# Kernel tuning notes

Hardware: AMD Instinct MI355X
Metric: run time of the kernel (lower is better)

## Reference

```python
import jax, jax.numpy as jnp
import numpy as np

N_TOKEN = 8192
N_EMBED = 512
N_SAMPLE = 10
TAU = 1.0
RHO = 1.0


def setup_inputs() -> dict:
    key = jax.random.key(0)
    k1, k2 = jax.random.split(key)
    inputs = jax.random.normal(k1, (4, 2048, N_EMBED), dtype=jnp.float32)
    embeds = jax.random.normal(k2, (N_TOKEN, N_EMBED), dtype=jnp.float32)
    return {"inputs": inputs, "embeds": embeds}


def reference(inputs, embeds):
    size = inputs.shape
    x = inputs.reshape(-1, N_EMBED)  # (N, D)
    n = x.shape[0]
    # squared distances, scaled by n_token (as in get_distances)
    dists = (jnp.sum(x * x, axis=-1, keepdims=True)
             + jnp.sum(embeds * embeds, axis=-1)[None, :]
             - 2.0 * jnp.matmul(x, embeds.T)) / N_TOKEN  # (N, K)
    logits = -dists / TAU  # categorical(softmax(logits)) == categorical(logits)
    skey = jax.random.fold_in(jax.random.key(0), 1)
    # multinomial with replacement: n_sample i.i.d. categorical draws per row
    samples = jax.random.categorical(skey, logits[:, None, :], axis=-1,
                                     shape=(n, N_SAMPLE))  # (N, n_sample) int
    quantized_embs = embeds[samples].mean(axis=1)  # (N, D) gather + mean
    quantized = x + jax.lax.stop_gradient(quantized_embs - x)  # straight-through
    gkey = jax.random.fold_in(jax.random.key(0), 2)
    gates = jax.random.bernoulli(gkey, RHO, (n,)).astype(x.dtype)[:, None]
    quantized = quantized * gates + (1.0 - gates) * x
    quantized = quantized.reshape(size)
    samples = samples.reshape(size[:-1] + (N_SAMPLE,))
    return quantized, samples
```

## Files before the change

### kernel.cpp

```cpp
#include <hip/hip_runtime.h>
#include <stdint.h>
#include <math.h>

#define N_ROWS 8192
#define N_TOK  8192
#define N_DIM  512
#define N_SAMP 10
#define GK     1536

typedef __attribute__((ext_vector_type(8))) short bf16x8_t;
typedef __attribute__((ext_vector_type(4))) float f32x4_t;

__host__ __device__ __forceinline__ void tf2x32(uint32_t ks0, uint32_t ks1,
                                                uint32_t& x0, uint32_t& x1) {
  uint32_t ks2 = ks0 ^ ks1 ^ 0x1BD11BDAu;
  x0 += ks0; x1 += ks1;
#define TF_ROUND(r) { x0 += x1; x1 = (x1 << (r)) | (x1 >> (32 - (r))); x1 ^= x0; }
  TF_ROUND(13) TF_ROUND(15) TF_ROUND(26) TF_ROUND(6)
  x0 += ks1; x1 += ks2 + 1u;
  TF_ROUND(17) TF_ROUND(29) TF_ROUND(16) TF_ROUND(24)
  x0 += ks2; x1 += ks0 + 2u;
  TF_ROUND(13) TF_ROUND(15) TF_ROUND(26) TF_ROUND(6)
  x0 += ks0; x1 += ks1 + 3u;
  TF_ROUND(17) TF_ROUND(29) TF_ROUND(16) TF_ROUND(24)
  x0 += ks1; x1 += ks2 + 4u;
  TF_ROUND(13) TF_ROUND(15) TF_ROUND(26) TF_ROUND(6)
  x0 += ks2; x1 += ks0 + 5u;
#undef TF_ROUND
}

__device__ __forceinline__ unsigned short f2bf_rne(float f) {
  uint32_t u = __float_as_uint(f);
  uint32_t r = (u + 0x7fffu + ((u >> 16) & 1u)) >> 16;
  return (unsigned short)r;
}
__device__ __forceinline__ float bf2f(unsigned short h) {
  return __uint_as_float((uint32_t)h << 16);
}

__global__ __launch_bounds__(256) void rownorm_kernel(const float* __restrict__ M,
                                                      float* __restrict__ out) {
  int lane = threadIdx.x & 63;
  int row = (int)((blockIdx.x * blockDim.x + threadIdx.x) >> 6);
  const float* p = M + (size_t)row * N_DIM;
  float acc = 0.f;
#pragma unroll
  for (int d = 0; d < N_DIM; d += 64) {
    float v = p[d + lane];
    acc = fmaf(v, v, acc);
  }
#pragma unroll
  for (int off = 32; off; off >>= 1) acc += __shfl_xor(acc, off, 64);
  if (lane == 0) out[row] = acc;
}

__global__ __launch_bounds__(256) void init_state_kernel(float* __restrict__ rmin,
                                                         int* __restrict__ ridx) {
  int i = blockIdx.x * 256 + threadIdx.x;
  if (i < N_ROWS * N_SAMP) { rmin[i] = INFINITY; ridx[i] = 0; }
}

__global__ __launch_bounds__(256) void split_kernel(const float* __restrict__ src,
                                                    unsigned short* __restrict__ dst,
                                                    int mode) {
  int t = blockIdx.x * 256 + threadIdx.x;
  int row = t >> 7;
  int c = (t & 127) << 2;
  float4 v = *(const float4*)(src + (size_t)row * N_DIM + c);
  ushort4 hi, lo;
  hi.x = f2bf_rne(v.x); lo.x = f2bf_rne(v.x - bf2f(hi.x));
  hi.y = f2bf_rne(v.y); lo.y = f2bf_rne(v.y - bf2f(hi.y));
  hi.z = f2bf_rne(v.z); lo.z = f2bf_rne(v.z - bf2f(hi.z));
  hi.w = f2bf_rne(v.w); lo.w = f2bf_rne(v.w - bf2f(hi.w));
  unsigned short* base = dst + (size_t)row * GK;
  *(ushort4*)(base + c) = hi;
  if (mode == 0) {
    *(ushort4*)(base + 512 + c) = lo;
    *(ushort4*)(base + 1024 + c) = hi;
  } else {
    *(ushort4*)(base + 512 + c) = hi;
    *(ushort4*)(base + 1024 + c) = lo;
  }
}

__device__ __forceinline__ void async_cp16(const void* g, void* l) {
  __builtin_amdgcn_global_load_lds((const __attribute__((address_space(1))) void*)g,
                                   (__attribute__((address_space(3))) void*)l, 16, 0, 0);
}

__global__ __launch_bounds__(256) void gemm_bf16_kernel(const unsigned short* __restrict__ A2,
                                                        const unsigned short* __restrict__ B2,
                                                        const float* __restrict__ xx,
                                                        const float* __restrict__ ee,
                                                        float* __restrict__ E,
                                                        int ks, int KC) {
  __shared__ __align__(16) unsigned short As[128 * 32];
  __shared__ __align__(16) unsigned short Bs[128 * 32];
  int tid = threadIdx.x;
  int w = tid >> 6, l = tid & 63;
  int row0 = blockIdx.y * 128;
  int col0 = blockIdx.x * 128;
  int bcol0 = ks + col0;
  int wm = (w & 1) * 64, wn = (w >> 1) * 64;
  int quad = l >> 4, r15 = l & 15;

  f32x4_t acc[4][4];
#pragma unroll
  for (int i = 0; i < 4; ++i)
#pragma unroll
    for (int j = 0; j < 4; ++j) acc[i][j] = (f32x4_t){0.f, 0.f, 0.f, 0.f};

  int c0 = w * 64 + l;
  int c1 = c0 + 256;
  const size_t ga0 = (size_t)(row0 + (c0 >> 2)) * GK + (c0 & 3) * 8;
  const size_t ga1 = (size_t)(row0 + (c1 >> 2)) * GK + (c1 & 3) * 8;
  const size_t gb0 = (size_t)(bcol0 + (c0 >> 2)) * GK + (c0 & 3) * 8;
  const size_t gb1 = (size_t)(bcol0 + (c1 >> 2)) * GK + (c1 & 3) * 8;

  for (int k0 = 0; k0 < GK; k0 += 32) {
    async_cp16(A2 + ga0 + k0, As + c0 * 8);
    async_cp16(A2 + ga1 + k0, As + c1 * 8);
    async_cp16(B2 + gb0 + k0, Bs + c0 * 8);
    async_cp16(B2 + gb1 + k0, Bs + c1 * 8);
    __syncthreads();

    bf16x8_t af[4], bf[4];
#pragma unroll
    for (int i = 0; i < 4; ++i)
      af[i] = *(const bf16x8_t*)&As[(wm + i * 16 + r15) * 32 + quad * 8];
#pragma unroll
    for (int j = 0; j < 4; ++j)
      bf[j] = *(const bf16x8_t*)&Bs[(wn + j * 16 + r15) * 32 + quad * 8];
#pragma unroll
    for (int i = 0; i < 4; ++i)
#pragma unroll
      for (int j = 0; j < 4; ++j)
        acc[i][j] = __builtin_amdgcn_mfma_f32_16x16x32_bf16(af[i], bf[j], acc[i][j], 0, 0, 0);
    __syncthreads();
  }

  const float inv_nt = 1.f / 8192.f;
  float eev[4];
#pragma unroll
  for (int j = 0; j < 4; ++j) eev[j] = ee[ks + col0 + wn + j * 16 + r15];
#pragma unroll
  for (int i = 0; i < 4; ++i) {
#pragma unroll
    for (int r = 0; r < 4; ++r) {
      int grow = row0 + wm + i * 16 + quad * 4 + r;
      float xxv = xx[grow];
#pragma unroll
      for (int j = 0; j < 4; ++j) {
        int gcol = col0 + wn + j * 16 + r15;
        float dist = (xxv + eev[j] - 2.0f * acc[i][j][r]) * inv_nt;
        E[(size_t)grow * KC + gcol] = expf(dist);
      }
    }
  }
}

__global__ __launch_bounds__(256) void gemm_nt_kernel(const float* __restrict__ A,
                                                      const float* __restrict__ B,
                                                      const float* __restrict__ xx,
                                                      const float* __restrict__ ee,
                                                      float* __restrict__ E,
                                                      int ks, int KC) {
  __shared__ __align__(16) float Asf[32][68];
  __shared__ __align__(16) float Bsf[32][68];
  int tid = threadIdx.x;
  int row0 = blockIdx.y * 64;
  int colB0 = blockIdx.x * 64 + ks;
  int tx = tid & 15, ty = tid >> 4;
  float acc[4][4] = {};
  for (int d0 = 0; d0 < N_DIM; d0 += 32) {
#pragma unroll
    for (int r = 0; r < 2; ++r) {
      int c = tid + 256 * r;
      int m = c >> 3;
      int dv = (c & 7) << 2;
      const float4 va = *(const float4*)(A + (size_t)(row0 + m) * N_DIM + d0 + dv);
      Asf[dv + 0][m] = va.x; Asf[dv + 1][m] = va.y;
      Asf[dv + 2][m] = va.z; Asf[dv + 3][m] = va.w;
      const float4 vb = *(const float4*)(B + (size_t)(colB0 + m) * N_DIM + d0 + dv);
      Bsf[dv + 0][m] = vb.x; Bsf[dv + 1][m] = vb.y;
      Bsf[dv + 2][m] = vb.z; Bsf[dv + 3][m] = vb.w;
    }
    __syncthreads();
#pragma unroll
    for (int dd = 0; dd < 32; ++dd) {
      float4 a4 = *(const float4*)&Asf[dd][ty << 2];
      float4 b4 = *(const float4*)&Bsf[dd][tx << 2];
      float av[4] = {a4.x, a4.y, a4.z, a4.w};
      float bv[4] = {b4.x, b4.y, b4.z, b4.w};
#pragma unroll
      for (int i = 0; i < 4; ++i)
#pragma unroll
        for (int j = 0; j < 4; ++j)
          acc[i][j] = fmaf(av[i], bv[j], acc[i][j]);
    }
    __syncthreads();
  }
  const float inv_nt = 1.f / 8192.f;
  int colC0 = blockIdx.x * 64;
  float eev[4];
#pragma unroll
  for (int j = 0; j < 4; ++j) eev[j] = ee[ks + colC0 + (tx << 2) + j];
#pragma unroll
  for (int i = 0; i < 4; ++i) {
    int grow = row0 + (ty << 2) + i;
    float xxv = xx[grow];
    float4 v;
    v.x = expf((xxv + eev[0] - 2.0f * acc[i][0]) * inv_nt);
    v.y = expf((xxv + eev[1] - 2.0f * acc[i][1]) * inv_nt);
    v.z = expf((xxv + eev[2] - 2.0f * acc[i][2]) * inv_nt);
    v.w = expf((xxv + eev[3] - 2.0f * acc[i][3]) * inv_nt);
    *(float4*)(E + (size_t)grow * KC + colC0 + (tx << 2)) = v;
  }
}

__global__ __launch_bounds__(256) void sample_kernel(const float* __restrict__ E,
                                                     float* __restrict__ rmin,
                                                     int* __restrict__ ridx,
                                                     int ks, int KC,
                                                     uint32_t k0, uint32_t k1) {
  int lane = threadIdx.x & 63;
  int row = (int)((blockIdx.x * blockDim.x + threadIdx.x) >> 6);
  float bmin[N_SAMP];
  int bidx[N_SAMP];
#pragma unroll
  for (int s = 0; s < N_SAMP; ++s) { bmin[s] = INFINITY; bidx[s] = 0; }
  const float tiny = 1.1754943508222875e-38f;
  uint32_t row_c = (uint32_t)row * (uint32_t)N_SAMP * 8192u;

  for (int kk = lane; kk < KC; kk += 64) {
    int k = ks + kk;
    float Ek = E[(size_t)row * KC + kk];
    uint32_t base_c = row_c + (uint32_t)k;
#pragma unroll
    for (int s = 0; s < N_SAMP; ++s) {
      uint32_t x0 = 0u, x1 = base_c + (uint32_t)s * 8192u;
      tf2x32(k0, k1, x0, x1);
      uint32_t bits = x0 ^ x1;
      float u = __uint_as_float(0x3f800000u | (bits >> 9)) - 1.0f;
      u = fmaxf(u, tiny);
      float wv = -logf(u) * Ek;
      if (wv < bmin[s]) { bmin[s] = wv; bidx[s] = k; }
    }
  }
#pragma unroll
  for (int s = 0; s < N_SAMP; ++s) {
    float v = bmin[s];
    int id = bidx[s];
#pragma unroll
    for (int off = 32; off; off >>= 1) {
      float ov = __shfl_xor(v, off, 64);
      int oi = __shfl_xor(id, off, 64);
      if (ov < v || (ov == v && oi < id)) { v = ov; id = oi; }
    }
    if (lane == 0) {
      size_t p = (size_t)row * N_SAMP + s;
      if (v < rmin[p]) { rmin[p] = v; ridx[p] = id; }
    }
  }
}

__global__ __launch_bounds__(256) void gather_kernel(const float* __restrict__ emb,
                                                     const int* __restrict__ ridx,
                                                     const float* __restrict__ x,
                                                     float* __restrict__ outq,
                                                     float* __restrict__ outs) {
  int lane = threadIdx.x & 63;
  int row = (int)((blockIdx.x * blockDim.x + threadIdx.x) >> 6);
  int idx[N_SAMP];
#pragma unroll
  for (int s = 0; s < N_SAMP; ++s) idx[s] = ridx[row * N_SAMP + s];
  if (lane < N_SAMP) outs[row * N_SAMP + lane] = (float)idx[lane];
#pragma unroll
  for (int c = lane; c < N_DIM; c += 64) {
    float sum = 0.f;
#pragma unroll
    for (int s = 0; s < N_SAMP; ++s) sum += emb[(size_t)idx[s] * N_DIM + c];
    float qe = sum / 10.0f;
    float xv = x[(size_t)row * N_DIM + c];
    outq[(size_t)row * N_DIM + c] = xv + (qe - xv);
  }
}

extern "C" void kernel_launch(void* const* d_in, const int* in_sizes, int n_in,
                              void* d_out, int out_size, void* d_ws, size_t ws_size,
                              hipStream_t stream) {
  const float* x = (const float*)d_in[0];
  const float* emb = (const float*)d_in[1];
  float* out_q = (float*)d_out;
  float* out_s = out_q + (size_t)N_ROWS * N_DIM;

  const size_t fixed_f = (size_t)N_ROWS + N_TOK + 2 * (size_t)N_ROWS * N_SAMP;
  const size_t out_f = (size_t)N_ROWS * N_DIM + (size_t)N_ROWS * N_SAMP;
  const size_t split_u = (size_t)N_ROWS * GK;

  uint32_t s0 = 0u, s1 = 1u;
  tf2x32(0u, 0u, s0, s1);

  int KC = 0;
  for (int c = 8192; c >= 128; c >>= 1) {
    size_t need = fixed_f * 4 + 2 * split_u * 2 + (size_t)N_ROWS * c * 4;
    if (need <= ws_size) { KC = c; break; }
  }

  if (KC) {
    float* xx = (float*)d_ws;
    float* ee = xx + N_ROWS;
    float* rmin = ee + N_TOK;
    int* ridx = (int*)(rmin + (size_t)N_ROWS * N_SAMP);
    unsigned short* A2 = (unsigned short*)(ridx + (size_t)N_ROWS * N_SAMP);
    unsigned short* B2 = A2 + split_u;
    float* E = (float*)(B2 + split_u);

    rownorm_kernel<<<2048, 256, 0, stream>>>(x, xx);
    rownorm_kernel<<<2048, 256, 0, stream>>>(emb, ee);
    init_state_kernel<<<(N_ROWS * N_SAMP + 255) / 256, 256, 0, stream>>>(rmin, ridx);
    split_kernel<<<N_ROWS * 128 / 256, 256, 0, stream>>>(x, A2, 0);
    split_kernel<<<N_ROWS * 128 / 256, 256, 0, stream>>>(emb, B2, 1);

    for (int ks = 0; ks < N_TOK; ks += KC) {
      gemm_bf16_kernel<<<dim3(KC / 128, N_ROWS / 128), 256, 0, stream>>>(A2, B2, xx, ee, E, ks, KC);
      sample_kernel<<<2048, 256, 0, stream>>>(E, rmin, ridx, ks, KC, s0, s1);
    }
    gather_kernel<<<2048, 256, 0, stream>>>(emb, ridx, x, out_q, out_s);
    return;
  }

  float *xx, *ee, *rmin, *E;
  int* ridx;
  KC = 0;
  for (int c = 8192; c >= 64; c >>= 1) {
    if ((fixed_f + (size_t)N_ROWS * c) * 4 <= ws_size) { KC = c; break; }
  }
  if (KC) {
    xx = (float*)d_ws;
    ee = xx + N_ROWS;
    rmin = ee + N_TOK;
    ridx = (int*)(rmin + (size_t)N_ROWS * N_SAMP);
    E = (float*)(ridx + (size_t)N_ROWS * N_SAMP);
  } else if (fixed_f * 4 <= ws_size) {
    KC = 512;
    xx = (float*)d_ws;
    ee = xx + N_ROWS;
    rmin = ee + N_TOK;
    ridx = (int*)(rmin + (size_t)N_ROWS * N_SAMP);
    E = out_q;
  } else {
    KC = 256;
    E = out_q;
    float* tail = out_q + (out_f - fixed_f);
    xx = tail;
    ee = xx + N_ROWS;
    rmin = ee + N_TOK;
    ridx = (int*)(rmin + (size_t)N_ROWS * N_SAMP);
  }

  rownorm_kernel<<<2048, 256, 0, stream>>>(x, xx);
  rownorm_kernel<<<2048, 256, 0, stream>>>(emb, ee);
  init_state_kernel<<<(N_ROWS * N_SAMP + 255) / 256, 256, 0, stream>>>(rmin, ridx);
  for (int ks = 0; ks < N_TOK; ks += KC) {
    gemm_nt_kernel<<<dim3(KC / 64, N_ROWS / 64), 256, 0, stream>>>(x, emb, xx, ee, E, ks, KC);
    sample_kernel<<<2048, 256, 0, stream>>>(E, rmin, ridx, ks, KC, s0, s1);
  }
  gather_kernel<<<2048, 256, 0, stream>>>(emb, ridx, x, out_q, out_s);
}
```

Before: 1.724 ms.

## Fuse distance GEMM with Gumbel-style sampling via packed 64-bit atomicMin

Sampling moves into the bf16 MFMA GEMM epilogue. Each tile computes exp(dist), generates the threefry randoms per element, reduces a packed (value,index) 64-bit key across 16 lanes, and merges the winners globally with atomicMin. This removes the 256 MB intermediate E matrix write and read, and launches a single 64x64-tile grid instead of chunked GEMM/sample pairs. In exchange the GEMM blocks carry the heavy RNG and log work in registers, and about 10 atomics per row per column tile contend on the same addresses. Sample indices are now unpacked in a separate kernel before the gather.

```diff
diff --git a/kernel.cpp b/kernel.cpp
--- a/kernel.cpp
+++ b/kernel.cpp
@@ -38,6 +38,13 @@
   return __uint_as_float((uint32_t)h << 16);
 }
 
+__device__ __forceinline__ unsigned long long shfl_xor_u64(unsigned long long v, int off) {
+  uint32_t lo = (uint32_t)v, hi = (uint32_t)(v >> 32);
+  lo = (uint32_t)__shfl_xor((int)lo, off, 64);
+  hi = (uint32_t)__shfl_xor((int)hi, off, 64);
+  return ((unsigned long long)hi << 32) | lo;
+}
+
 __global__ __launch_bounds__(256) void rownorm_kernel(const float* __restrict__ M,
                                                       float* __restrict__ out) {
   int lane = threadIdx.x & 63;
@@ -54,10 +61,9 @@
   if (lane == 0) out[row] = acc;
 }
 
-__global__ __launch_bounds__(256) void init_state_kernel(float* __restrict__ rmin,
-                                                         int* __restrict__ ridx) {
+__global__ __launch_bounds__(256) void init_pack_kernel(unsigned long long* __restrict__ rpack) {
   int i = blockIdx.x * 256 + threadIdx.x;
-  if (i < N_ROWS * N_SAMP) { rmin[i] = INFINITY; ridx[i] = 0; }
+  if (i < N_ROWS * N_SAMP) rpack[i] = 0xFFFFFFFFFFFFFFFFULL;
 }
 
 __global__ __launch_bounds__(256) void split_kernel(const float* __restrict__ src,
@@ -88,19 +94,16 @@
                                    (__attribute__((address_space(3))) void*)l, 16, 0, 0);
 }
 
-__global__ __launch_bounds__(256) void gemm_bf16_kernel(const unsigned short* __restrict__ A2,
-                                                        const unsigned short* __restrict__ B2,
-                                                        const float* __restrict__ xx,
-                                                        const float* __restrict__ ee,
-                                                        float* __restrict__ E,
-                                                        int ks, int KC) {
+__global__ __launch_bounds__(256) void fused_gemm_sample_kernel(
+    const unsigned short* __restrict__ A2, const unsigned short* __restrict__ B2,
+    const float* __restrict__ xx, const float* __restrict__ ee,
+    unsigned long long* __restrict__ rpack, uint32_t k0s, uint32_t k1s) {
   __shared__ __align__(16) unsigned short As[128 * 32];
   __shared__ __align__(16) unsigned short Bs[128 * 32];
   int tid = threadIdx.x;
   int w = tid >> 6, l = tid & 63;
   int row0 = blockIdx.y * 128;
   int col0 = blockIdx.x * 128;
-  int bcol0 = ks + col0;
   int wm = (w & 1) * 64, wn = (w >> 1) * 64;
   int quad = l >> 4, r15 = l & 15;
 
@@ -114,8 +117,8 @@
   int c1 = c0 + 256;
   const size_t ga0 = (size_t)(row0 + (c0 >> 2)) * GK + (c0 & 3) * 8;
   const size_t ga1 = (size_t)(row0 + (c1 >> 2)) * GK + (c1 & 3) * 8;
-  const size_t gb0 = (size_t)(bcol0 + (c0 >> 2)) * GK + (c0 & 3) * 8;
-  const size_t gb1 = (size_t)(bcol0 + (c1 >> 2)) * GK + (c1 & 3) * 8;
+  const size_t gb0 = (size_t)(col0 + (c0 >> 2)) * GK + (c0 & 3) * 8;
+  const size_t gb1 = (size_t)(col0 + (c1 >> 2)) * GK + (c1 & 3) * 8;
 
   for (int k0 = 0; k0 < GK; k0 += 32) {
     async_cp16(A2 + ga0 + k0, As + c0 * 8);
@@ -142,18 +145,51 @@
   const float inv_nt = 1.f / 8192.f;
   float eev[4];
 #pragma unroll
-  for (int j = 0; j < 4; ++j) eev[j] = ee[ks + col0 + wn + j * 16 + r15];
+  for (int j = 0; j < 4; ++j) eev[j] = ee[col0 + wn + j * 16 + r15];
 #pragma unroll
   for (int i = 0; i < 4; ++i) {
 #pragma unroll
     for (int r = 0; r < 4; ++r) {
-      int grow = row0 + wm + i * 16 + quad * 4 + r;
-      float xxv = xx[grow];
-#pragma unroll
-      for (int j = 0; j < 4; ++j) {
-        int gcol = col0 + wn + j * 16 + r15;
-        float dist = (xxv + eev[j] - 2.0f * acc[i][j][r]) * inv_nt;
-        E[(size_t)grow * KC + gcol] = expf(dist);
+      float xxv = xx[row0 + wm + i * 16 + quad * 4 + r];
+#pragma unroll
+      for (int j = 0; j < 4; ++j)
+        acc[i][j][r] = expf((xxv + eev[j] - 2.0f * acc[i][j][r]) * inv_nt);
+    }
+  }
+
+  const float tiny = 1.1754943508222875e-38f;
+  uint32_t kcol[4];
+#pragma unroll
+  for (int j = 0; j < 4; ++j) kcol[j] = (uint32_t)(col0 + wn + j * 16 + r15);
+  int rbase = row0 + wm + quad * 4;
+
+  for (int s = 0; s < N_SAMP; ++s) {
+    uint32_t soff = (uint32_t)s * 8192u;
+#pragma unroll
+    for (int i = 0; i < 4; ++i) {
+#pragma unroll
+      for (int r = 0; r < 4; ++r) {
+        uint32_t rowid = (uint32_t)(rbase + i * 16 + r);
+        uint32_t cbase = rowid * 81920u + soff;
+        unsigned long long b = 0xFFFFFFFFFFFFFFFFULL;
+#pragma unroll
+        for (int j = 0; j < 4; ++j) {
+          uint32_t x0 = 0u, x1 = cbase + kcol[j];
+          tf2x32(k0s, k1s, x0, x1);
+          uint32_t bits = x0 ^ x1;
+          float u = __uint_as_float(0x3f800000u | (bits >> 9)) - 1.0f;
+          u = fmaxf(u, tiny);
+          float wv = -logf(u) * acc[i][j][r];
+          unsigned long long p =
+              ((unsigned long long)__float_as_uint(wv) << 32) | kcol[j];
+          b = (p < b) ? p : b;
+        }
+#pragma unroll
+        for (int off = 1; off < 16; off <<= 1) {
+          unsigned long long ob = shfl_xor_u64(b, off);
+          b = (ob < b) ? ob : b;
+        }
+        if (r15 == 0) atomicMin(&rpack[(size_t)rowid * N_SAMP + s], b);
       }
     }
   }
@@ -219,23 +255,21 @@
 }
 
 __global__ __launch_bounds__(256) void sample_kernel(const float* __restrict__ E,
-                                                     float* __restrict__ rmin,
-                                                     int* __restrict__ ridx,
+                                                     unsigned long long* __restrict__ rpack,
                                                      int ks, int KC,
                                                      uint32_t k0, uint32_t k1) {
   int lane = threadIdx.x & 63;
   int row = (int)((blockIdx.x * blockDim.x + threadIdx.x) >> 6);
-  float bmin[N_SAMP];
-  int bidx[N_SAMP];
-#pragma unroll
-  for (int s = 0; s < N_SAMP; ++s) { bmin[s] = INFINITY; bidx[s] = 0; }
+  unsigned long long best[N_SAMP];
+#pragma unroll
+  for (int s = 0; s < N_SAMP; ++s) best[s] = 0xFFFFFFFFFFFFFFFFULL;
   const float tiny = 1.1754943508222875e-38f;
-  uint32_t row_c = (uint32_t)row * (uint32_t)N_SAMP * 8192u;
+  uint32_t row_c = (uint32_t)row * 81920u;
 
   for (int kk = lane; kk < KC; kk += 64) {
-    int k = ks + kk;
+    uint32_t k = (uint32_t)(ks + kk);
     float Ek = E[(size_t)row * KC + kk];
-    uint32_t base_c = row_c + (uint32_t)k;
+    uint32_t base_c = row_c + k;
 #pragma unroll
     for (int s = 0; s < N_SAMP; ++s) {
       uint32_t x0 = 0u, x1 = base_c + (uint32_t)s * 8192u;
@@ -244,37 +278,37 @@
       float u = __uint_as_float(0x3f800000u | (bits >> 9)) - 1.0f;
       u = fmaxf(u, tiny);
       float wv = -logf(u) * Ek;
-      if (wv < bmin[s]) { bmin[s] = wv; bidx[s] = k; }
+      unsigned long long p = ((unsigned long long)__float_as_uint(wv) << 32) | k;
+      if (p < best[s]) best[s] = p;
     }
   }
 #pragma unroll
   for (int s = 0; s < N_SAMP; ++s) {
-    float v = bmin[s];
-    int id = bidx[s];
+    unsigned long long b = best[s];
 #pragma unroll
     for (int off = 32; off; off >>= 1) {
-      float ov = __shfl_xor(v, off, 64);
-      int oi = __shfl_xor(id, off, 64);
-      if (ov < v || (ov == v && oi < id)) { v = ov; id = oi; }
-    }
-    if (lane == 0) {
-      size_t p = (size_t)row * N_SAMP + s;
-      if (v < rmin[p]) { rmin[p] = v; ridx[p] = id; }
-    }
-  }
+      unsigned long long ob = shfl_xor_u64(b, off);
+      b = (ob < b) ? ob : b;
+    }
+    if (lane == 0) atomicMin(&rpack[(size_t)row * N_SAMP + s], b);
+  }
+}
+
+__global__ __launch_bounds__(256) void unpack_kernel(const unsigned long long* __restrict__ rpack,
+                                                     float* __restrict__ outs) {
+  int i = blockIdx.x * 256 + threadIdx.x;
+  if (i < N_ROWS * N_SAMP) outs[i] = (float)(uint32_t)(rpack[i] & 0xFFFFFFFFu);
 }
 
 __global__ __launch_bounds__(256) void gather_kernel(const float* __restrict__ emb,
-                                                     const int* __restrict__ ridx,
+                                                     const float* __restrict__ outs,
                                                      const float* __restrict__ x,
-                                                     float* __restrict__ outq,
-                                                     float* __restrict__ outs) {
+                                                     float* __restrict__ outq) {
   int lane = threadIdx.x & 63;
   int row = (int)((blockIdx.x * blockDim.x + threadIdx.x) >> 6);
   int idx[N_SAMP];
 #pragma unroll
-  for (int s = 0; s < N_SAMP; ++s) idx[s] = ridx[row * N_SAMP + s];
-  if (lane < N_SAMP) outs[row * N_SAMP + lane] = (float)idx[lane];
+  for (int s = 0; s < N_SAMP; ++s) idx[s] = (int)outs[row * N_SAMP + s];
 #pragma unroll
   for (int c = lane; c < N_DIM; c += 64) {
     float sum = 0.f;
@@ -294,77 +328,65 @@
   float* out_q = (float*)d_out;
   float* out_s = out_q + (size_t)N_ROWS * N_DIM;
 
-  const size_t fixed_f = (size_t)N_ROWS + N_TOK + 2 * (size_t)N_ROWS * N_SAMP;
-  const size_t out_f = (size_t)N_ROWS * N_DIM + (size_t)N_ROWS * N_SAMP;
+  const size_t pack_n = (size_t)N_ROWS * N_SAMP;
+  const size_t fixed_b = (N_ROWS + N_TOK) * 4 + pack_n * 8;
   const size_t split_u = (size_t)N_ROWS * GK;
 
   uint32_t s0 = 0u, s1 = 1u;
   tf2x32(0u, 0u, s0, s1);
 
-  int KC = 0;
-  for (int c = 8192; c >= 128; c >>= 1) {
-    size_t need = fixed_f * 4 + 2 * split_u * 2 + (size_t)N_ROWS * c * 4;
-    if (need <= ws_size) { KC = c; break; }
-  }
-
-  if (KC) {
+  if (fixed_b + 2 * split_u * 2 <= ws_size) {
     float* xx = (float*)d_ws;
     float* ee = xx + N_ROWS;
-    float* rmin = ee + N_TOK;
-    int* ridx = (int*)(rmin + (size_t)N_ROWS * N_SAMP);
-    unsigned short* A2 = (unsigned short*)(ridx + (size_t)N_ROWS * N_SAMP);
+    unsigned long long* rpack = (unsigned long long*)(ee + N_TOK);
+    unsigned short* A2 = (unsigned short*)(rpack + pack_n);
     unsigned short* B2 = A2 + split_u;
-    float* E = (float*)(B2 + split_u);
 
     rownorm_kernel<<<2048, 256, 0, stream>>>(x, xx);
     rownorm_kernel<<<2048, 256, 0, stream>>>(emb, ee);
-    init_state_kernel<<<(N_ROWS * N_SAMP + 255) / 256, 256, 0, stream>>>(rmin, ridx);
+    init_pack_kernel<<<(int)((pack_n + 255) / 256), 256, 0, stream>>>(rpack);
     split_kernel<<<N_ROWS * 128 / 256, 256, 0, stream>>>(x, A2, 0);
     split_kernel<<<N_ROWS * 128 / 256, 256, 0, stream>>>(emb, B2, 1);
 
-    for (int ks = 0; ks < N_TOK; ks += KC) {
-      gemm_bf16_kernel<<<dim3(KC / 128, N_ROWS / 128), 256, 0, stream>>>(A2, B2, xx, ee, E, ks, KC);
-      sample_kernel<<<2048, 256, 0, stream>>>(E, rmin, ridx, ks, KC, s0, s1);
-    }
-    gather_kernel<<<2048, 256, 0, stream>>>(emb, ridx, x, out_q, out_s);
+    fused_gemm_sample_kernel<<<dim3(64, 64), 256, 0, stream>>>(A2, B2, xx, ee, rpack, s0, s1);
+
+    unpack_kernel<<<(int)((pack_n + 255) / 256), 256, 0, stream>>>(rpack, out_s);
+    gather_kernel<<<2048, 256, 0, stream>>>(emb, out_s, x, out_q);
     return;
   }
 
-  float *xx, *ee, *rmin, *E;
-  int* ridx;
-  KC = 0;
+  float *xx, *ee, *E;
+  unsigned long long* rpack;
+  int KC = 0;
   for (int c = 8192; c >= 64; c >>= 1) {
-    if ((fixed_f + (size_t)N_ROWS * c) * 4 <= ws_size) { KC = c; break; }
+    if (fixed_b + (size_t)N_ROWS * c * 4 <= ws_size) { KC = c; break; }
   }
   if (KC) {
     xx = (float*)d_ws;
     ee = xx + N_ROWS;
-    rmin = ee + N_TOK;
-    ridx = (int*)(rmin + (size_t)N_ROWS * N_SAMP);
-    E = (float*)(ridx + (size_t)N_ROWS * N_SAMP);
-  } else if (fixed_f * 4 <= ws_size) {
+    rpack = (unsigned long long*)(ee + N_TOK);
+    E = (float*)(rpack + pack_n);
+  } else if (fixed_b <= ws_size) {
     KC = 512;
     xx = (float*)d_ws;
     ee = xx + N_ROWS;
-    rmin = ee + N_TOK;
-    ridx = (int*)(rmin + (size_t)N_ROWS * N_SAMP);
+    rpack = (unsigned long long*)(ee + N_TOK);
     E = out_q;
   } else {
     KC = 256;
     E = out_q;
-    float* tail = out_q + (out_f - fixed_f);
-    xx = tail;
+    rpack = (unsigned long long*)(out_q + (size_t)N_ROWS * 256);
+    xx = (float*)(rpack + pack_n);
     ee = xx + N_ROWS;
-    rmin = ee + N_TOK;
-    ridx = (int*)(rmin + (size_t)N_ROWS * N_SAMP);
   }
 
   rownorm_kernel<<<2048, 256, 0, stream>>>(x, xx);
   rownorm_kernel<<<2048, 256, 0, stream>>>(emb, ee);
-  init_state_kernel<<<(N_ROWS * N_SAMP + 255) / 256, 256, 0, stream>>>(rmin, ridx);
+  init_pack_kernel<<<(int)((pack_n + 255) / 256), 256, 0, stream>>>(rpack);
   for (int ks = 0; ks < N_TOK; ks += KC) {
     gemm_nt_kernel<<<dim3(KC / 64, N_ROWS / 64), 256, 0, stream>>>(x, emb, xx, ee, E, ks, KC);
-    sample_kernel<<<2048, 256, 0, stream>>>(E, rmin, ridx, ks, KC, s0, s1);
-  }
-  gather_kernel<<<2048, 256, 0, stream>>>(emb, ridx, x, out_q, out_s);
-}
+    sample_kernel<<<2048, 256, 0, stream>>>(E, rpack, ks, KC, s0, s1);
+  }
+  unpack_kernel<<<(int)((pack_n + 255) / 256), 256, 0, stream>>>(rpack, out_s);
+  gather_kernel<<<2048, 256, 0, stream>>>(emb, out_s, x, out_q);
+}
```

After: 1.813 ms. 5.2% more time.
